# Performance work log

Hardware: AMD Instinct MI355X
Metric: run time of the kernel (lower is better)

The kernel has to match this reference:

```python
import jax, jax.numpy as jnp
import numpy as np

N_NODES = 100000
N_EDGES = 800000
IN_FEATS = 128
HIDDEN = 64
SCALE = 0.5 ** 0.5  # sqrt(0.5) residual scale
BN_EPS = 1e-5


def setup_inputs() -> dict:
    key = jax.random.key(0)
    ks = jax.random.split(key, 12)
    return {
        "src": jax.random.randint(ks[0], (N_EDGES,), 0, N_NODES, dtype=jnp.int64)
        if jax.config.jax_enable_x64 else jax.random.randint(ks[0], (N_EDGES,), 0, N_NODES),
        "dst": jax.random.randint(ks[1], (N_EDGES,), 0, N_NODES),
        "x": jax.random.normal(ks[2], (N_NODES, IN_FEATS), dtype=jnp.float32),
        "fc_w": jax.random.normal(ks[3], (IN_FEATS, HIDDEN), dtype=jnp.float32) * 0.05,
        "fc_b": jax.random.normal(ks[4], (HIDDEN,), dtype=jnp.float32) * 0.05,
        "w1": jax.random.normal(ks[5], (HIDDEN, HIDDEN), dtype=jnp.float32) * 0.05,
        "b1": jax.random.normal(ks[6], (HIDDEN,), dtype=jnp.float32) * 0.05,
        "w2": jax.random.normal(ks[7], (HIDDEN, HIDDEN), dtype=jnp.float32) * 0.05,
        "b2": jax.random.normal(ks[8], (HIDDEN,), dtype=jnp.float32) * 0.05,
        "gamma": jax.random.normal(ks[9], (HIDDEN,), dtype=jnp.float32) * 0.05 + 1.0,
        "beta": jax.random.normal(ks[10], (HIDDEN,), dtype=jnp.float32) * 0.05,
    }


def _graph_conv(h, w, b, src, dst, norm_src, norm_dst, n_nodes):
    # DGL GraphConv, norm='both': y = D_in^{-1/2} A D_out^{-1/2} (h W) + b
    h = h @ w                                   # [N, H]
    m = h[src] * norm_src[:, None]              # gather + src-degree norm, [E, H]
    agg = jax.ops.segment_sum(m, dst, num_segments=n_nodes)  # scatter-add, [N, H]
    return agg * norm_dst[:, None] + b


def reference(src, dst, x, fc_w, fc_b, w1, b1, w2, b2, gamma, beta):
    n_nodes = x.shape[0]
    ones_e = jnp.ones(src.shape[0], dtype=x.dtype)
    deg_out = jnp.clip(jax.ops.segment_sum(ones_e, src, num_segments=n_nodes), 1.0)
    deg_in = jnp.clip(jax.ops.segment_sum(ones_e, dst, num_segments=n_nodes), 1.0)
    norm_src = (deg_out ** -0.5)[src]           # per-edge source normalization
    norm_dst = deg_in ** -0.5                   # per-node destination normalization

    h = x @ fc_w + fc_b                          # fc: [N, H]
    h = (h + _graph_conv(h, w1, b1, src, dst, norm_src, norm_dst, n_nodes)) * SCALE
    h = (h + _graph_conv(h, w2, b2, src, dst, norm_src, norm_dst, n_nodes)) * SCALE

    # BatchNorm1d (training-mode batch statistics over nodes, biased variance)
    mu = h.mean(axis=0)
    var = ((h - mu) ** 2).mean(axis=0)
    h = (h - mu) * jax.lax.rsqrt(var + BN_EPS) * gamma + beta
    return h
```

## Files before the change

### kernel.cpp

```cpp
#include <hip/hip_runtime.h>

#define HIDDEN 64
#define INFEAT 128
#define SCALE_C 0.70710678118654752f
#define BN_EPS 1e-5f
#define AGG_GRID 2048
#define RED_BLK 32

__device__ __forceinline__ int rli(int v, int l){ return __builtin_amdgcn_readlane(v, l); }
__device__ __forceinline__ float rlf(float v, int l){
  return __int_as_float(__builtin_amdgcn_readlane(__float_as_int(v), l));
}

template<int KDIM, bool ADDB, bool FUSET>
__device__ __forceinline__ void gemm_body(int bid, const float* __restrict__ X,
    const float* __restrict__ W, const float* __restrict__ B,
    float* __restrict__ Y, const float* __restrict__ W2, float* __restrict__ T, int N)
{
  __shared__ float smem[64 * 65];
  const int tid  = threadIdx.x;
  const int lane = tid & 63;
  const int wid  = __builtin_amdgcn_readfirstlane(tid >> 6);
  const int c0 = wid * 16;
  const int base = bid * 64;
  const int gnode = base + lane;

  float acc[16];
  #pragma unroll
  for (int c = 0; c < 16; ++c) acc[c] = ADDB ? B[c0 + c] : 0.f;

  constexpr int NCHUNK = KDIM / 32;
  #pragma unroll 1
  for (int ck = 0; ck < NCHUNK; ++ck){
    __syncthreads();
    #pragma unroll
    for (int i = 0; i < 2; ++i){
      int f  = i * 256 + tid;
      int nd = f >> 3;
      int kq = f & 7;
      float4 v = make_float4(0.f, 0.f, 0.f, 0.f);
      if (base + nd < N)
        v = *(const float4*)(X + (size_t)(base + nd) * KDIM + ck * 32 + kq * 4);
      float* p = &smem[nd * 65 + kq * 4];
      p[0] = v.x; p[1] = v.y; p[2] = v.z; p[3] = v.w;
    }
    __syncthreads();
    const float* wrow = W + (size_t)ck * 32 * HIDDEN + c0;
    #pragma unroll
    for (int k = 0; k < 32; ++k){
      float xv = smem[lane * 65 + k];
      #pragma unroll
      for (int c = 0; c < 16; ++c)
        acc[c] = fmaf(xv, wrow[k * HIDDEN + c], acc[c]);
    }
  }

  if (gnode < N){
    float4* yp = (float4*)(Y + (size_t)gnode * HIDDEN + c0);
    #pragma unroll
    for (int j = 0; j < 4; ++j)
      yp[j] = make_float4(acc[4*j], acc[4*j+1], acc[4*j+2], acc[4*j+3]);
  }

  if constexpr (FUSET){
    __syncthreads();
    #pragma unroll
    for (int c = 0; c < 16; ++c) smem[lane * 65 + c0 + c] = acc[c];
    __syncthreads();
    float tacc[16];
    #pragma unroll
    for (int c = 0; c < 16; ++c) tacc[c] = 0.f;
    const float* w2r = W2 + c0;
    #pragma unroll
    for (int k = 0; k < 64; ++k){
      float hv = smem[lane * 65 + k];
      #pragma unroll
      for (int c = 0; c < 16; ++c)
        tacc[c] = fmaf(hv, w2r[k * HIDDEN + c], tacc[c]);
    }
    if (gnode < N){
      float4* tp = (float4*)(T + (size_t)gnode * HIDDEN + c0);
      #pragma unroll
      for (int j = 0; j < 4; ++j)
        tp[j] = make_float4(tacc[4*j], tacc[4*j+1], tacc[4*j+2], tacc[4*j+3]);
    }
  }
}

__device__ __forceinline__ int role_gemm_idx(int b, int GB, int TOT, int& histIdx){
  int fb  = (int)(((long)b * GB) / TOT);
  int fb1 = (int)(((long)(b + 1) * GB) / TOT);
  histIdx = b - fb;
  return (fb1 > fb) ? fb : -1;
}

__global__ __launch_bounds__(256) void k_mega1(const int* __restrict__ dst,
    int* __restrict__ degI, int* __restrict__ rank, int E,
    const float* __restrict__ x, const float* __restrict__ fc_w,
    const float* __restrict__ fc_b, float* __restrict__ h,
    const float* __restrict__ w1, float* __restrict__ t, int N, int GB, int TOT){
  int hIdx;
  int g = role_gemm_idx(blockIdx.x, GB, TOT, hIdx);
  if (g >= 0) gemm_body<INFEAT, true, true>(g, x, fc_w, fc_b, h, w1, t, N);
  else {
    int e0 = hIdx * 1024 + threadIdx.x;
    #pragma unroll
    for (int i = 0; i < 4; ++i){
      int e = e0 + i * 256;
      if (e < E) rank[e] = atomicAdd(&degI[dst[e]], 1);
    }
  }
}

__global__ __launch_bounds__(256) void k_place(const int* __restrict__ src,
    const int* __restrict__ dst, const int* __restrict__ rank,
    const int* __restrict__ rp, int* __restrict__ cs, int* __restrict__ degO, int E){
  int e0 = blockIdx.x * 1024 + threadIdx.x;
  #pragma unroll
  for (int i = 0; i < 4; ++i){
    int e = e0 + i * 256;
    if (e < E){
      int s = src[e];
      cs[rp[dst[e]] + rank[e]] = s;
      atomicAdd(&degO[s], 1);
    }
  }
}

__global__ __launch_bounds__(256) void k_gemm64(const float* __restrict__ X,
    const float* __restrict__ W, float* __restrict__ Y, int N){
  gemm_body<HIDDEN, false, false>(blockIdx.x, X, W, nullptr, Y, nullptr, nullptr, N);
}

__global__ void k_scan1(const int* __restrict__ deg, int* __restrict__ bsum, int N){
  __shared__ int sh[256];
  int t = threadIdx.x;
  int i = blockIdx.x * 256 + t;
  sh[t] = (i < N) ? deg[i] : 0;
  __syncthreads();
  for (int ofs = 128; ofs > 0; ofs >>= 1){
    if (t < ofs) sh[t] += sh[t + ofs];
    __syncthreads();
  }
  if (t == 0) bsum[blockIdx.x] = sh[0];
}

__global__ void k_scan2(int* __restrict__ bsum, int NB){
  __shared__ int sh[512];
  int t = threadIdx.x;
  int v = (t < NB) ? bsum[t] : 0;
  sh[t] = v;
  __syncthreads();
  for (int ofs = 1; ofs < 512; ofs <<= 1){
    int u = (t >= ofs) ? sh[t - ofs] : 0;
    __syncthreads();
    sh[t] += u;
    __syncthreads();
  }
  if (t < NB) bsum[t] = sh[t] - v;
}

__global__ void k_scan3(const int* __restrict__ degI, const int* __restrict__ bofs,
                        int* __restrict__ rp, float* __restrict__ norm_in, int N, int E){
  __shared__ int sh[256];
  int t = threadIdx.x;
  int i = blockIdx.x * 256 + t;
  int v = (i < N) ? degI[i] : 0;
  sh[t] = v;
  __syncthreads();
  for (int ofs = 1; ofs < 256; ofs <<= 1){
    int u = (t >= ofs) ? sh[t - ofs] : 0;
    __syncthreads();
    sh[t] += u;
    __syncthreads();
  }
  if (i < N){
    int excl = sh[t] - v + bofs[blockIdx.x];
    rp[i] = excl;
    if (i == N - 1) rp[N] = E;
    norm_in[i] = rsqrtf((float)max(v, 1));
  }
}

template<bool PRE>
__device__ __forceinline__ float4 gather_row4(const int* __restrict__ rp,
    const int* __restrict__ cs, const float* __restrict__ t,
    const int* __restrict__ degO, int n, int g, int s4){
  const int start = rp[n], end = rp[n + 1];
  float4 acc = make_float4(0.f, 0.f, 0.f, 0.f);
  int j = start + g;
  for (; j + 4 < end; j += 8){
    int a0 = cs[j], a1 = cs[j + 4];
    float4 v0 = *(const float4*)(t + (size_t)a0 * HIDDEN + s4);
    float4 v1 = *(const float4*)(t + (size_t)a1 * HIDDEN + s4);
    if (PRE){
      acc.x += v0.x; acc.y += v0.y; acc.z += v0.z; acc.w += v0.w;
      acc.x += v1.x; acc.y += v1.y; acc.z += v1.z; acc.w += v1.w;
    } else {
      float n0 = rsqrtf((float)degO[a0]);
      float n1 = rsqrtf((float)degO[a1]);
      acc.x = fmaf(v0.x, n0, acc.x); acc.y = fmaf(v0.y, n0, acc.y);
      acc.z = fmaf(v0.z, n0, acc.z); acc.w = fmaf(v0.w, n0, acc.w);
      acc.x = fmaf(v1.x, n1, acc.x); acc.y = fmaf(v1.y, n1, acc.y);
      acc.z = fmaf(v1.z, n1, acc.z); acc.w = fmaf(v1.w, n1, acc.w);
    }
  }
  if (j < end){
    int a = cs[j];
    float4 v = *(const float4*)(t + (size_t)a * HIDDEN + s4);
    if (PRE){
      acc.x += v.x; acc.y += v.y; acc.z += v.z; acc.w += v.w;
    } else {
      float nn = rsqrtf((float)degO[a]);
      acc.x = fmaf(v.x, nn, acc.x); acc.y = fmaf(v.y, nn, acc.y);
      acc.z = fmaf(v.z, nn, acc.z); acc.w = fmaf(v.w, nn, acc.w);
    }
  }
  return acc;
}

__device__ __forceinline__ float4 xreduce4(float4 a){
  #pragma unroll
  for (int m = 16; m <= 32; m <<= 1){
    a.x += __shfl_xor(a.x, m, 64);
    a.y += __shfl_xor(a.y, m, 64);
    a.z += __shfl_xor(a.z, m, 64);
    a.w += __shfl_xor(a.w, m, 64);
  }
  return a;
}

template<bool BN, bool PRE, bool FUSET2>
__global__ __launch_bounds__(256, 4) void k_agg(const int* __restrict__ rp, const int* __restrict__ cs,
    const float* __restrict__ t, const int* __restrict__ degO,
    const float* __restrict__ norm_in, const float* __restrict__ b,
    const float* __restrict__ w2, float* __restrict__ h,
    float* __restrict__ t2, float* __restrict__ bnpart, int N)
{
  const int tid  = threadIdx.x;
  const int lane = tid & 63;
  const int g    = lane >> 4;
  const int s    = lane & 15;
  const int s4   = s * 4;
  const int wv = (blockIdx.x * 256 + tid) >> 6;
  const int nw = (gridDim.x * 256) >> 6;
  const float4 bv = ((const float4*)b)[s];
  float4 s1 = make_float4(0.f,0.f,0.f,0.f), s2 = make_float4(0.f,0.f,0.f,0.f);

  float w2c[64];
  if constexpr (FUSET2){
    #pragma unroll
    for (int k = 0; k < 64; ++k) w2c[k] = w2[k * HIDDEN + lane];
  }

  for (int n = wv; n < N; n += nw){
    float4 acc = gather_row4<PRE>(rp, cs, t, degO, n, g, s4);
    acc = xreduce4(acc);
    const size_t rowo = (size_t)n * HIDDEN;
    const float4 hv = *(const float4*)(h + rowo + s4);
    const float ni = norm_in[n];
    float4 v;
    v.x = (hv.x + acc.x * ni + bv.x) * SCALE_C;
    v.y = (hv.y + acc.y * ni + bv.y) * SCALE_C;
    v.z = (hv.z + acc.z * ni + bv.z) * SCALE_C;
    v.w = (hv.w + acc.w * ni + bv.w) * SCALE_C;
    if (g == 0){
      *(float4*)(h + rowo + s4) = v;
      if (BN){
        s1.x += v.x; s1.y += v.y; s1.z += v.z; s1.w += v.w;
        s2.x += v.x*v.x; s2.y += v.y*v.y; s2.z += v.z*v.z; s2.w += v.w*v.w;
      }
    }
    if constexpr (FUSET2){
      float nout = rsqrtf((float)max(degO[n], 1));
      float ta0 = 0.f, ta1 = 0.f, ta2 = 0.f, ta3 = 0.f;
      #pragma unroll
      for (int k = 0; k < 64; k += 4){
        const int ln = k >> 2;
        ta0 = fmaf(rlf(v.x, ln), w2c[k],     ta0);
        ta1 = fmaf(rlf(v.y, ln), w2c[k + 1], ta1);
        ta2 = fmaf(rlf(v.z, ln), w2c[k + 2], ta2);
        ta3 = fmaf(rlf(v.w, ln), w2c[k + 3], ta3);
      }
      t2[rowo + lane] = ((ta0 + ta1) + (ta2 + ta3)) * nout;
    }
  }

  if (BN){
    __shared__ float l1[4][64], l2[4][64];
    const int wid = tid >> 6;
    if (g == 0){
      l1[wid][s4+0] = s1.x; l1[wid][s4+1] = s1.y; l1[wid][s4+2] = s1.z; l1[wid][s4+3] = s1.w;
      l2[wid][s4+0] = s2.x; l2[wid][s4+1] = s2.y; l2[wid][s4+2] = s2.z; l2[wid][s4+3] = s2.w;
    }
    __syncthreads();
    if (tid < 64){
      float a1 = l1[0][tid] + l1[1][tid] + l1[2][tid] + l1[3][tid];
      float a2 = l2[0][tid] + l2[1][tid] + l2[2][tid] + l2[3][tid];
      bnpart[blockIdx.x * 128 + tid] = a1;
      bnpart[blockIdx.x * 128 + 64 + tid] = a2;
    }
  }
}

__global__ __launch_bounds__(256) void k_bnred(const float* __restrict__ bnpart,
    float* __restrict__ bnred, int nblk){
  int col  = threadIdx.x & 127;
  int half = threadIdx.x >> 7;
  int rows = nblk / RED_BLK;
  int r0 = blockIdx.x * rows;
  float s = 0.f;
  for (int r = half; r < rows; r += 2)
    s += bnpart[(size_t)(r0 + r) * 128 + col];
  __shared__ float sh[256];
  sh[threadIdx.x] = s;
  __syncthreads();
  if (threadIdx.x < 128)
    bnred[blockIdx.x * 128 + threadIdx.x] = sh[threadIdx.x] + sh[threadIdx.x + 128];
}

__global__ void k_bnfin(const float* __restrict__ bnred,
    const float* __restrict__ gamma, const float* __restrict__ beta,
    float* __restrict__ bnab, float invN){
  int c = threadIdx.x;
  float s1 = 0.f, s2 = 0.f;
  #pragma unroll
  for (int b = 0; b < RED_BLK; ++b){ s1 += bnred[b*128 + c]; s2 += bnred[b*128 + 64 + c]; }
  float mu  = s1 * invN;
  float var = s2 * invN - mu * mu;
  float rstd = rsqrtf(var + BN_EPS);
  float sc = gamma[c] * rstd;
  bnab[c] = sc;
  bnab[64 + c] = beta[c] - mu * sc;
}

__global__ void k_bnapply(float* __restrict__ h, const float* __restrict__ bnab, long total4){
  long i = (long)blockIdx.x * blockDim.x + threadIdx.x;
  if (i < total4){
    int c = (int)((i * 4) & 63);
    float4 v = ((float4*)h)[i];
    v.x = fmaf(v.x, bnab[c],     bnab[64 + c]);
    v.y = fmaf(v.y, bnab[c + 1], bnab[65 + c]);
    v.z = fmaf(v.z, bnab[c + 2], bnab[66 + c]);
    v.w = fmaf(v.w, bnab[c + 3], bnab[67 + c]);
    ((float4*)h)[i] = v;
  }
}

extern "C" void kernel_launch(void* const* d_in, const int* in_sizes, int n_in,
                              void* d_out, int out_size, void* d_ws, size_t ws_size,
                              hipStream_t stream){
  const int* src = (const int*)d_in[0];
  const int* dst = (const int*)d_in[1];
  const float* x     = (const float*)d_in[2];
  const float* fc_w  = (const float*)d_in[3];
  const float* fc_b  = (const float*)d_in[4];
  const float* w1    = (const float*)d_in[5];
  const float* b1    = (const float*)d_in[6];
  const float* w2    = (const float*)d_in[7];
  const float* b2    = (const float*)d_in[8];
  const float* gamma = (const float*)d_in[9];
  const float* beta  = (const float*)d_in[10];
  const int E = in_sizes[0];
  const int N = in_sizes[2] / INFEAT;
  const int NB  = (N + 255) / 256;
  const int EB4 = (E + 1023) / 1024;
  const int GB  = (N + 63) / 64;
  const int TOT = EB4 + GB;

  float* h = (float*)d_out;

  const size_t Nh = (size_t)N * HIDDEN;
  size_t need = (2 * Nh + N + (size_t)AGG_GRID * 128 + RED_BLK * 128 + 128) * 4
              + ((size_t)3 * N + 1 + 512 + 2 * (size_t)E) * 4;
  const bool fused = ws_size >= need;

  float* t        = (float*)d_ws;
  float* t2       = fused ? (t + Nh) : nullptr;
  float* norm_in  = fused ? (t2 + Nh) : (t + Nh);
  float* bnpart   = norm_in + N;
  float* bnred    = bnpart + AGG_GRID * 128;
  float* bnab     = bnred + RED_BLK * 128;
  int*   degO     = (int*)(bnab + 128);
  int*   degI     = degO + N;
  int*   rp       = degI + N;
  int*   bsum     = rp + N + 1;
  int*   rank     = bsum + 512;
  int*   cs       = rank + E;

  hipMemsetAsync(degO, 0, 2 * (size_t)N * sizeof(int), stream);

  k_mega1<<<TOT, 256, 0, stream>>>(dst, degI, rank, E,
                                   x, fc_w, fc_b, h, w1, t, N, GB, TOT);

  k_scan1<<<NB, 256, 0, stream>>>(degI, bsum, N);
  k_scan2<<<1, 512, 0, stream>>>(bsum, NB);
  k_scan3<<<NB, 256, 0, stream>>>(degI, bsum, rp, norm_in, N, E);

  k_place<<<EB4, 256, 0, stream>>>(src, dst, rank, rp, cs, degO, E);

  if (fused){
    k_agg<false, false, true><<<AGG_GRID, 256, 0, stream>>>(
        rp, cs, t, degO, norm_in, b1, w2, h, t2, nullptr, N);
    k_agg<true, true, false><<<AGG_GRID, 256, 0, stream>>>(
        rp, cs, t2, degO, norm_in, b2, nullptr, h, nullptr, bnpart, N);
  } else {
    k_agg<false, false, false><<<AGG_GRID, 256, 0, stream>>>(
        rp, cs, t, degO, norm_in, b1, nullptr, h, nullptr, nullptr, N);
    k_gemm64<<<GB, 256, 0, stream>>>(h, w2, t, N);
    k_agg<true, false, false><<<AGG_GRID, 256, 0, stream>>>(
        rp, cs, t, degO, norm_in, b2, nullptr, h, nullptr, bnpart, N);
  }

  k_bnred<<<RED_BLK, 256, 0, stream>>>(bnpart, bnred, AGG_GRID);
  k_bnfin<<<1, 64, 0, stream>>>(bnred, gamma, beta, bnab, 1.0f / (float)N);
  long total4 = (long)N * HIDDEN / 4;
  k_bnapply<<<(int)((total4 + 255) / 256), 256, 0, stream>>>(h, bnab, total4);
}
```

Measured before the change: 341.0 us.

## Process two nodes per wave in aggregation and move W2 to LDS

The aggregation kernel now gathers two destination nodes at once, interleaving their neighbor loads with predicated weights so more independent memory requests are in flight per wave. The fused second-layer transform reads W2 from shared memory instead of a 64-register per-lane array, which frees registers to hold the extra accumulators. The edge-histogram and placement kernels also handle 8 edges per thread instead of 4, halving their block counts. The dual loop runs until the longer of the two neighbor lists ends, so lanes waste work on masked loads when degrees differ. The padded loads hit index 0.

```diff
diff --git a/kernel.cpp b/kernel.cpp
--- a/kernel.cpp
+++ b/kernel.cpp
@@ -103,9 +103,9 @@
   int g = role_gemm_idx(blockIdx.x, GB, TOT, hIdx);
   if (g >= 0) gemm_body<INFEAT, true, true>(g, x, fc_w, fc_b, h, w1, t, N);
   else {
-    int e0 = hIdx * 1024 + threadIdx.x;
-    #pragma unroll
-    for (int i = 0; i < 4; ++i){
+    int e0 = hIdx * 2048 + threadIdx.x;
+    #pragma unroll
+    for (int i = 0; i < 8; ++i){
       int e = e0 + i * 256;
       if (e < E) rank[e] = atomicAdd(&degI[dst[e]], 1);
     }
@@ -115,9 +115,9 @@
 __global__ __launch_bounds__(256) void k_place(const int* __restrict__ src,
     const int* __restrict__ dst, const int* __restrict__ rank,
     const int* __restrict__ rp, int* __restrict__ cs, int* __restrict__ degO, int E){
-  int e0 = blockIdx.x * 1024 + threadIdx.x;
+  int e0 = blockIdx.x * 2048 + threadIdx.x;
   #pragma unroll
-  for (int i = 0; i < 4; ++i){
+  for (int i = 0; i < 8; ++i){
     int e = e0 + i * 256;
     if (e < E){
       int s = src[e];
@@ -183,40 +183,43 @@
 }
 
 template<bool PRE>
-__device__ __forceinline__ float4 gather_row4(const int* __restrict__ rp,
+__device__ __forceinline__ void gather_dual(const int* __restrict__ rp,
     const int* __restrict__ cs, const float* __restrict__ t,
-    const int* __restrict__ degO, int n, int g, int s4){
-  const int start = rp[n], end = rp[n + 1];
-  float4 acc = make_float4(0.f, 0.f, 0.f, 0.f);
-  int j = start + g;
-  for (; j + 4 < end; j += 8){
-    int a0 = cs[j], a1 = cs[j + 4];
-    float4 v0 = *(const float4*)(t + (size_t)a0 * HIDDEN + s4);
-    float4 v1 = *(const float4*)(t + (size_t)a1 * HIDDEN + s4);
-    if (PRE){
-      acc.x += v0.x; acc.y += v0.y; acc.z += v0.z; acc.w += v0.w;
-      acc.x += v1.x; acc.y += v1.y; acc.z += v1.z; acc.w += v1.w;
-    } else {
-      float n0 = rsqrtf((float)degO[a0]);
-      float n1 = rsqrtf((float)degO[a1]);
-      acc.x = fmaf(v0.x, n0, acc.x); acc.y = fmaf(v0.y, n0, acc.y);
-      acc.z = fmaf(v0.z, n0, acc.z); acc.w = fmaf(v0.w, n0, acc.w);
-      acc.x = fmaf(v1.x, n1, acc.x); acc.y = fmaf(v1.y, n1, acc.y);
-      acc.z = fmaf(v1.z, n1, acc.z); acc.w = fmaf(v1.w, n1, acc.w);
-    }
-  }
-  if (j < end){
-    int a = cs[j];
-    float4 v = *(const float4*)(t + (size_t)a * HIDDEN + s4);
-    if (PRE){
-      acc.x += v.x; acc.y += v.y; acc.z += v.z; acc.w += v.w;
-    } else {
-      float nn = rsqrtf((float)degO[a]);
-      acc.x = fmaf(v.x, nn, acc.x); acc.y = fmaf(v.y, nn, acc.y);
-      acc.z = fmaf(v.z, nn, acc.z); acc.w = fmaf(v.w, nn, acc.w);
-    }
-  }
-  return acc;
+    const int* __restrict__ degO, int nA, int nB, int g, int s4,
+    float4& outA, float4& outB)
+{
+  const int sA = rp[nA], eA = rp[nA + 1];
+  const int sB = (nB >= 0) ? rp[nB] : 0;
+  const int eB = (nB >= 0) ? rp[nB + 1] : 0;
+  float4 aA = make_float4(0.f, 0.f, 0.f, 0.f);
+  float4 aB = make_float4(0.f, 0.f, 0.f, 0.f);
+  int jA = sA + g, jB = sB + g;
+  while (jA < eA || jB < eB){
+    const int j0 = jA, j1 = jA + 4, j2 = jB, j3 = jB + 4;
+    const int c0 = (j0 < eA) ? j0 : 0;
+    const int c1 = (j1 < eA) ? j1 : 0;
+    const int c2 = (j2 < eB) ? j2 : 0;
+    const int c3 = (j3 < eB) ? j3 : 0;
+    const int i0 = cs[c0], i1 = cs[c1], i2 = cs[c2], i3 = cs[c3];
+    const float4 v0 = *(const float4*)(t + (size_t)i0 * HIDDEN + s4);
+    const float4 v1 = *(const float4*)(t + (size_t)i1 * HIDDEN + s4);
+    const float4 v2 = *(const float4*)(t + (size_t)i2 * HIDDEN + s4);
+    const float4 v3 = *(const float4*)(t + (size_t)i3 * HIDDEN + s4);
+    const float w0 = (j0 < eA) ? (PRE ? 1.f : rsqrtf((float)degO[i0])) : 0.f;
+    const float w1 = (j1 < eA) ? (PRE ? 1.f : rsqrtf((float)degO[i1])) : 0.f;
+    const float w2 = (j2 < eB) ? (PRE ? 1.f : rsqrtf((float)degO[i2])) : 0.f;
+    const float w3 = (j3 < eB) ? (PRE ? 1.f : rsqrtf((float)degO[i3])) : 0.f;
+    aA.x = fmaf(v0.x, w0, aA.x); aA.y = fmaf(v0.y, w0, aA.y);
+    aA.z = fmaf(v0.z, w0, aA.z); aA.w = fmaf(v0.w, w0, aA.w);
+    aA.x = fmaf(v1.x, w1, aA.x); aA.y = fmaf(v1.y, w1, aA.y);
+    aA.z = fmaf(v1.z, w1, aA.z); aA.w = fmaf(v1.w, w1, aA.w);
+    aB.x = fmaf(v2.x, w2, aB.x); aB.y = fmaf(v2.y, w2, aB.y);
+    aB.z = fmaf(v2.z, w2, aB.z); aB.w = fmaf(v2.w, w2, aB.w);
+    aB.x = fmaf(v3.x, w3, aB.x); aB.y = fmaf(v3.y, w3, aB.y);
+    aB.z = fmaf(v3.z, w3, aB.z); aB.w = fmaf(v3.w, w3, aB.w);
+    jA += 8; jB += 8;
+  }
+  outA = aA; outB = aB;
 }
 
 __device__ __forceinline__ float4 xreduce4(float4 a){
@@ -247,42 +250,75 @@
   const float4 bv = ((const float4*)b)[s];
   float4 s1 = make_float4(0.f,0.f,0.f,0.f), s2 = make_float4(0.f,0.f,0.f,0.f);
 
-  float w2c[64];
+  __shared__ float w2l[FUSET2 ? (HIDDEN * HIDDEN) : 1];
   if constexpr (FUSET2){
-    #pragma unroll
-    for (int k = 0; k < 64; ++k) w2c[k] = w2[k * HIDDEN + lane];
-  }
-
-  for (int n = wv; n < N; n += nw){
-    float4 acc = gather_row4<PRE>(rp, cs, t, degO, n, g, s4);
-    acc = xreduce4(acc);
-    const size_t rowo = (size_t)n * HIDDEN;
-    const float4 hv = *(const float4*)(h + rowo + s4);
-    const float ni = norm_in[n];
-    float4 v;
-    v.x = (hv.x + acc.x * ni + bv.x) * SCALE_C;
-    v.y = (hv.y + acc.y * ni + bv.y) * SCALE_C;
-    v.z = (hv.z + acc.z * ni + bv.z) * SCALE_C;
-    v.w = (hv.w + acc.w * ni + bv.w) * SCALE_C;
+    for (int i = tid; i < HIDDEN * HIDDEN; i += 256) w2l[i] = w2[i];
+  }
+  __syncthreads();
+
+  for (int n = wv; n < N; n += 2 * nw){
+    const int nB = (n + nw < N) ? (n + nw) : -1;
+    float4 accA, accB;
+    gather_dual<PRE>(rp, cs, t, degO, n, nB, g, s4, accA, accB);
+    accA = xreduce4(accA);
+    accB = xreduce4(accB);
+
+    const size_t roA = (size_t)n * HIDDEN;
+    const float niA = norm_in[n];
+    const float4 hA = *(const float4*)(h + roA + s4);
+    float4 vA;
+    vA.x = (hA.x + accA.x * niA + bv.x) * SCALE_C;
+    vA.y = (hA.y + accA.y * niA + bv.y) * SCALE_C;
+    vA.z = (hA.z + accA.z * niA + bv.z) * SCALE_C;
+    vA.w = (hA.w + accA.w * niA + bv.w) * SCALE_C;
+
+    size_t roB = 0; float4 vB = make_float4(0.f,0.f,0.f,0.f);
+    if (nB >= 0){
+      roB = (size_t)nB * HIDDEN;
+      const float niB = norm_in[nB];
+      const float4 hB = *(const float4*)(h + roB + s4);
+      vB.x = (hB.x + accB.x * niB + bv.x) * SCALE_C;
+      vB.y = (hB.y + accB.y * niB + bv.y) * SCALE_C;
+      vB.z = (hB.z + accB.z * niB + bv.z) * SCALE_C;
+      vB.w = (hB.w + accB.w * niB + bv.w) * SCALE_C;
+    }
+
     if (g == 0){
-      *(float4*)(h + rowo + s4) = v;
+      *(float4*)(h + roA + s4) = vA;
+      if (nB >= 0) *(float4*)(h + roB + s4) = vB;
       if (BN){
-        s1.x += v.x; s1.y += v.y; s1.z += v.z; s1.w += v.w;
-        s2.x += v.x*v.x; s2.y += v.y*v.y; s2.z += v.z*v.z; s2.w += v.w*v.w;
+        s1.x += vA.x; s1.y += vA.y; s1.z += vA.z; s1.w += vA.w;
+        s2.x += vA.x*vA.x; s2.y += vA.y*vA.y; s2.z += vA.z*vA.z; s2.w += vA.w*vA.w;
+        if (nB >= 0){
+          s1.x += vB.x; s1.y += vB.y; s1.z += vB.z; s1.w += vB.w;
+          s2.x += vB.x*vB.x; s2.y += vB.y*vB.y; s2.z += vB.z*vB.z; s2.w += vB.w*vB.w;
+        }
       }
     }
+
     if constexpr (FUSET2){
-      float nout = rsqrtf((float)max(degO[n], 1));
-      float ta0 = 0.f, ta1 = 0.f, ta2 = 0.f, ta3 = 0.f;
+      const float noA = rsqrtf((float)max(degO[n], 1));
+      const float noB = (nB >= 0) ? rsqrtf((float)max(degO[nB], 1)) : 0.f;
+      float a0 = 0.f, a1 = 0.f, a2 = 0.f, a3 = 0.f;
+      float b0 = 0.f, b1 = 0.f, b2 = 0.f, b3 = 0.f;
       #pragma unroll
       for (int k = 0; k < 64; k += 4){
         const int ln = k >> 2;
-        ta0 = fmaf(rlf(v.x, ln), w2c[k],     ta0);
-        ta1 = fmaf(rlf(v.y, ln), w2c[k + 1], ta1);
-        ta2 = fmaf(rlf(v.z, ln), w2c[k + 2], ta2);
-        ta3 = fmaf(rlf(v.w, ln), w2c[k + 3], ta3);
+        const float wk0 = w2l[(k    ) * HIDDEN + lane];
+        const float wk1 = w2l[(k + 1) * HIDDEN + lane];
+        const float wk2 = w2l[(k + 2) * HIDDEN + lane];
+        const float wk3 = w2l[(k + 3) * HIDDEN + lane];
+        a0 = fmaf(rlf(vA.x, ln), wk0, a0);
+        a1 = fmaf(rlf(vA.y, ln), wk1, a1);
+        a2 = fmaf(rlf(vA.z, ln), wk2, a2);
+        a3 = fmaf(rlf(vA.w, ln), wk3, a3);
+        b0 = fmaf(rlf(vB.x, ln), wk0, b0);
+        b1 = fmaf(rlf(vB.y, ln), wk1, b1);
+        b2 = fmaf(rlf(vB.z, ln), wk2, b2);
+        b3 = fmaf(rlf(vB.w, ln), wk3, b3);
       }
-      t2[rowo + lane] = ((ta0 + ta1) + (ta2 + ta3)) * nout;
+      t2[roA + lane] = ((a0 + a1) + (a2 + a3)) * noA;
+      if (nB >= 0) t2[roB + lane] = ((b0 + b1) + (b2 + b3)) * noB;
     }
   }
 
@@ -364,9 +400,9 @@
   const int E = in_sizes[0];
   const int N = in_sizes[2] / INFEAT;
   const int NB  = (N + 255) / 256;
-  const int EB4 = (E + 1023) / 1024;
+  const int EB8 = (E + 2047) / 2048;
   const int GB  = (N + 63) / 64;
-  const int TOT = EB4 + GB;
+  const int TOT = EB8 + GB;
 
   float* h = (float*)d_out;
 
@@ -397,7 +433,7 @@
   k_scan2<<<1, 512, 0, stream>>>(bsum, NB);
   k_scan3<<<NB, 256, 0, stream>>>(degI, bsum, rp, norm_in, N, E);
 
-  k_place<<<EB4, 256, 0, stream>>>(src, dst, rank, rp, cs, degO, E);
+  k_place<<<EB8, 256, 0, stream>>>(src, dst, rank, rp, cs, degO, E);
 
   if (fused){
     k_agg<false, false, true><<<AGG_GRID, 256, 0, stream>>>(
```

After: 350.9 us. 2.9% more time.
